# Kernel optimization log

Hardware: AMD Instinct MI355X
Metric: run time of the kernel (lower is better)

## Reference

```python
import jax, jax.numpy as jnp
import numpy as np

N_NODES = 50000
N_EDGES = 800000
IN_DIM = 256
OUT_DIM = 64
HEADS = 8


def setup_inputs() -> dict:
    key = jax.random.key(0)
    k1, k2, k3, k4, k5 = jax.random.split(key, 5)
    x = jax.random.normal(k1, (N_NODES, IN_DIM), dtype=jnp.float32)
    edge_index = jax.random.randint(k2, (2, N_EDGES), 0, N_NODES, dtype=jnp.int32)
    W = jax.random.normal(k3, (HEADS, IN_DIM, OUT_DIM), dtype=jnp.float32) / np.sqrt(IN_DIM)
    b = jnp.zeros((HEADS, OUT_DIM), dtype=jnp.float32)
    a = jax.random.normal(k4, (HEADS, 2 * OUT_DIM), dtype=jnp.float32)
    gate = jnp.ones((HEADS,), dtype=jnp.float32)
    return {"x": x, "edge_index": edge_index, "W": W, "b": b, "a": a, "gate": gate}


def reference(x, edge_index, W, b, a, gate):
    # Wh: [H, N, O] -- per-head linear projections
    Wh = jnp.einsum('nd,hdo->hno', x, W) + b[:, None, :]
    row, col = edge_index[0], edge_index[1]
    O = Wh.shape[-1]
    a_src, a_dst = a[:, :O], a[:, O:]  # split of concat weight: [H, O] each
    # score per edge per head: leaky_relu(cat(Wh[row], Wh[col]) @ a)
    e = (jnp.einsum('heo,ho->he', Wh[:, row], a_src)
         + jnp.einsum('heo,ho->he', Wh[:, col], a_dst))  # [H, E]
    e = jax.nn.leaky_relu(e, negative_slope=0.01)
    # NOTE: original code softmaxes over ALL edges (dim=0), not per node
    alpha = jax.nn.softmax(e, axis=1)  # [H, E]
    msgs = alpha[:, :, None] * Wh[:, col, :]  # [H, E, O]
    out = jax.vmap(lambda m: jax.ops.segment_sum(m, row, num_segments=Wh.shape[1]))(msgs)  # [H, N, O]
    g = jax.nn.softmax(gate)
    return jnp.einsum('h,hno->no', g, out)
```

## Files before the change

### kernel.cpp

```cpp
#include <hip/hip_runtime.h>
#include <hip/hip_bf16.h>


#define N_NODES 50000
#define N_EDGES 800000
#define IN_DIM  256
#define OUT_DIM 64
#define HEADS   8
#define NCOL    (HEADS * OUT_DIM)
#define NBLK_RED 1024
#define LN_W_EPS (-20.72326584f)

typedef __attribute__((ext_vector_type(8))) short short8;
typedef __attribute__((ext_vector_type(4))) float f32x4;

__device__ __forceinline__ void bf16_split2(float x0, float x1,
                                            unsigned& hi, unsigned& lo)
{
    unsigned u0 = __float_as_uint(x0), u1 = __float_as_uint(x1);
    unsigned r0 = u0 + 0x7FFFu + ((u0 >> 16) & 1u);
    unsigned r1 = u1 + 0x7FFFu + ((u1 >> 16) & 1u);
    float h0 = __uint_as_float(r0 & 0xFFFF0000u);
    float h1 = __uint_as_float(r1 & 0xFFFF0000u);
    hi = (r0 >> 16) | (r1 & 0xFFFF0000u);
    unsigned l0 = __float_as_uint(x0 - h0);
    unsigned l1 = __float_as_uint(x1 - h1);
    lo = (l0 >> 16) | (l1 & 0xFFFF0000u);
}

__global__ __launch_bounds__(256) void packw_kernel(
    const float* __restrict__ W, short* __restrict__ wp)
{
    const int ct = blockIdx.x;
    const int h  = ct >> 2;
    #pragma unroll
    for (int it = 0; it < 2; ++it) {
        const int i  = threadIdx.x + it * 256;
        const int k8 = i >> 4;
        const int c  = i & 15;
        const int o  = (ct & 3) * 16 + c;
        const float* src = W + (size_t)h * IN_DIM * OUT_DIM
                             + (size_t)k8 * 8 * OUT_DIM + o;
        unsigned hi[4], lo[4];
        #pragma unroll
        for (int p = 0; p < 4; ++p) {
            float x0 = src[(2 * p) * OUT_DIM];
            float x1 = src[(2 * p + 1) * OUT_DIM];
            bf16_split2(x0, x1, hi[p], lo[p]);
        }
        uint4 vh = make_uint4(hi[0], hi[1], hi[2], hi[3]);
        uint4 vl = make_uint4(lo[0], lo[1], lo[2], lo[3]);
        *(uint4*)(wp + (((size_t)(ct * 2 + 0) * 32 + k8) * 128) + c * 8) = vh;
        *(uint4*)(wp + (((size_t)(ct * 2 + 1) * 32 + k8) * 128) + c * 8) = vl;
    }
}

__global__ __launch_bounds__(512, 4) void gemm_kernel(
    const float* __restrict__ x, const short* __restrict__ wp,
    const float* __restrict__ b, const float* __restrict__ a,
    float* __restrict__ Wh, float* __restrict__ s_src, float* __restrict__ s_dst)
{
    __shared__ __align__(16) short As[32768];

    const int row0 = blockIdx.x * 64;
    const int tid  = threadIdx.x;
    const int lane = tid & 63;
    const int head = tid >> 6;
    const int r16  = lane & 15;
    const int kq   = lane >> 4;

    const short* pB = wp + (size_t)kq * 128 + (size_t)r16 * 8;
    #define LD_B(ni, s, ks) \
        (*(const short8*)(pB + ((((size_t)(head * 4 + (ni)) * 2 + (s)) * 32 + 4 * (ks)) * 128)))
    short8 Bh[2][4], Bl[2][4];
    #pragma unroll
    for (int ni = 0; ni < 4; ++ni) { Bh[0][ni] = LD_B(ni, 0, 0); Bl[0][ni] = LD_B(ni, 1, 0); }

    #pragma unroll
    for (int q = 0; q < 4; ++q) {
        const int item = q * 512 + tid;
        const int row  = item >> 5;
        const int kc   = item & 31;
        const int grow = row0 + row;
        f32x4 v0 = {0.f, 0.f, 0.f, 0.f}, v1 = {0.f, 0.f, 0.f, 0.f};
        if (grow < N_NODES) {
            v0 = *(const f32x4*)(x + (size_t)grow * IN_DIM + kc * 8);
            v1 = *(const f32x4*)(x + (size_t)grow * IN_DIM + kc * 8 + 4);
        }
        unsigned hi[4], lo[4];
        bf16_split2(v0.x, v0.y, hi[0], lo[0]);
        bf16_split2(v0.z, v0.w, hi[1], lo[1]);
        bf16_split2(v1.x, v1.y, hi[2], lo[2]);
        bf16_split2(v1.z, v1.w, hi[3], lo[3]);
        const int mi  = row >> 4, rr = row & 15;
        const int swz = rr ^ (kc & 15);
        uint4 vh = make_uint4(hi[0], hi[1], hi[2], hi[3]);
        uint4 vl = make_uint4(lo[0], lo[1], lo[2], lo[3]);
        *(uint4*)((char*)As + ((((mi * 2 + 0) * 32 + kc) * 16 + swz) * 16)) = vh;
        *(uint4*)((char*)As + ((((mi * 2 + 1) * 32 + kc) * 16 + swz) * 16)) = vl;
    }
    __syncthreads();

    f32x4 acc[4][4] = {};

    #define LD_A(mi, s, ks) \
        (*(const short8*)((const char*)As + \
            (((((mi) * 2 + (s)) * 32 + (4 * (ks) + kq)) * 16 + \
              (r16 ^ ((4 * ((ks) & 3) + kq)))) * 16)))

    short8 Ah[2][4], Al[2][4];
    #pragma unroll
    for (int mi = 0; mi < 4; ++mi) { Ah[0][mi] = LD_A(mi, 0, 0); Al[0][mi] = LD_A(mi, 1, 0); }

    #pragma unroll
    for (int ks = 0; ks < 8; ++ks) {
        const int cur = ks & 1, nxt = cur ^ 1;
        if (ks < 7) {
            #pragma unroll
            for (int ni = 0; ni < 4; ++ni) {
                Bh[nxt][ni] = LD_B(ni, 0, ks + 1);
                Bl[nxt][ni] = LD_B(ni, 1, ks + 1);
            }
            #pragma unroll
            for (int mi = 0; mi < 4; ++mi) {
                Ah[nxt][mi] = LD_A(mi, 0, ks + 1);
                Al[nxt][mi] = LD_A(mi, 1, ks + 1);
            }
        }
        #pragma unroll
        for (int mi = 0; mi < 4; ++mi)
            #pragma unroll
            for (int ni = 0; ni < 4; ++ni) {
                acc[mi][ni] = __builtin_amdgcn_mfma_f32_16x16x32_bf16(
                    Ah[cur][mi], Bh[cur][ni], acc[mi][ni], 0, 0, 0);
                acc[mi][ni] = __builtin_amdgcn_mfma_f32_16x16x32_bf16(
                    Ah[cur][mi], Bl[cur][ni], acc[mi][ni], 0, 0, 0);
                acc[mi][ni] = __builtin_amdgcn_mfma_f32_16x16x32_bf16(
                    Al[cur][mi], Bh[cur][ni], acc[mi][ni], 0, 0, 0);
            }
    }
    #undef LD_A
    #undef LD_B

    const int n0 = head * 64;
    float bias[4], avs[4], avd[4];
    #pragma unroll
    for (int ni = 0; ni < 4; ++ni) {
        bias[ni] = b[n0 + ni * 16 + r16];
        avs[ni]  = a[head * 128 + ni * 16 + r16];
        avd[ni]  = a[head * 128 + 64 + ni * 16 + r16];
    }
    #pragma unroll
    for (int mi = 0; mi < 4; ++mi) {
        #pragma unroll
        for (int reg = 0; reg < 4; ++reg) {
            const int r = row0 + mi * 16 + kq * 4 + reg;
            float v[4], ps = 0.f, pd = 0.f;
            #pragma unroll
            for (int ni = 0; ni < 4; ++ni) {
                v[ni] = acc[mi][ni][reg] + bias[ni];
                ps += v[ni] * avs[ni];
                pd += v[ni] * avd[ni];
            }
            if (r < N_NODES) {
                *(float4*)(Wh + (size_t)r * NCOL + n0 + r16 * 4) =
                    make_float4(v[0], v[1], v[2], v[3]);
            }
            ps += __shfl_xor(ps, 1); pd += __shfl_xor(pd, 1);
            ps += __shfl_xor(ps, 2); pd += __shfl_xor(pd, 2);
            ps += __shfl_xor(ps, 4); pd += __shfl_xor(pd, 4);
            ps += __shfl_xor(ps, 8); pd += __shfl_xor(pd, 8);
            if (r16 == 0 && r < N_NODES) {
                s_src[r * 8 + head] = ps;
                s_dst[r * 8 + head] = pd;
            }
        }
    }
}

__global__ __launch_bounds__(256) void edge_score_kernel(
    const int* __restrict__ ei, const float* __restrict__ s_src,
    const float* __restrict__ s_dst, float* __restrict__ tbuf,
    float* __restrict__ partial)
{
    const int tid  = threadIdx.x;
    const int half = tid & 1;

    float m[4], l[4];
    #pragma unroll
    for (int i = 0; i < 4; ++i) { m[i] = -1e30f; l[i] = 0.f; }

    for (int p = blockIdx.x * 128 + (tid >> 1); p < N_EDGES; p += gridDim.x * 128) {
        const int row = ei[p];
        const int col = ei[N_EDGES + p];
        const f32x4 s = *(const f32x4*)(s_src + row * 8 + half * 4);
        const f32x4 d = *(const f32x4*)(s_dst + col * 8 + half * 4);
        float t[4];
        #pragma unroll
        for (int i = 0; i < 4; ++i) {
            float v = s[i] + d[i];
            t[i] = v > 0.f ? v : 0.01f * v;
        }
        if (tbuf)
            *(float4*)(tbuf + (size_t)p * 8 + half * 4) =
                make_float4(t[0], t[1], t[2], t[3]);
        #pragma unroll
        for (int i = 0; i < 4; ++i) {
            const float mn = fmaxf(m[i], t[i]);
            l[i] = l[i] * __expf(m[i] - mn) + __expf(t[i] - mn);
            m[i] = mn;
        }
    }

    __shared__ float red[8][256];
    #pragma unroll
    for (int i = 0; i < 4; ++i) { red[i][tid] = m[i]; red[4 + i][tid] = l[i]; }
    __syncthreads();
    for (int s = 128; s >= 2; s >>= 1) {
        if (tid < s) {
            #pragma unroll
            for (int i = 0; i < 4; ++i) {
                const float mo = red[i][tid + s], lo = red[4 + i][tid + s];
                const float mm = red[i][tid],     ll = red[4 + i][tid];
                const float mn = fmaxf(mm, mo);
                red[4 + i][tid] = ll * __expf(mm - mn) + lo * __expf(mo - mn);
                red[i][tid]     = mn;
            }
        }
        __syncthreads();
    }
    if (tid < 2) {
        #pragma unroll
        for (int i = 0; i < 4; ++i) {
            partial[blockIdx.x * 16 + tid * 4 + i]     = red[i][tid];
            partial[blockIdx.x * 16 + 8 + tid * 4 + i] = red[4 + i][tid];
        }
    }
}

__global__ __launch_bounds__(256) void finalize_kernel(
    const float* __restrict__ partial, const float* __restrict__ gate,
    float* __restrict__ coef, int nblk)
{
    const int t = threadIdx.x;
    const int h = t & 7;
    const int j = t >> 3;
    float m = -1e30f, l = 0.f;
    for (int bk = j; bk < nblk; bk += 32) {
        const float mb = partial[bk * 16 + h];
        const float lb = partial[bk * 16 + 8 + h];
        const float mn = fmaxf(m, mb);
        l = l * __expf(m - mn) + lb * __expf(mb - mn);
        m = mn;
    }
    __shared__ float rm[256], rl[256];
    rm[t] = m; rl[t] = l;
    __syncthreads();
    for (int s = 128; s >= 8; s >>= 1) {
        if (t < s) {
            const float mo = rm[t + s], lo = rl[t + s];
            const float mn = fmaxf(rm[t], mo);
            rl[t] = rl[t] * __expf(rm[t] - mn) + lo * __expf(mo - mn);
            rm[t] = mn;
        }
        __syncthreads();
    }
    if (t < 8) {
        float gm = gate[0];
        for (int i = 1; i < 8; ++i) gm = fmaxf(gm, gate[i]);
        float gs = 0.f;
        for (int i = 0; i < 8; ++i) gs += __expf(gate[i] - gm);
        const float g = __expf(gate[t] - gm) / gs;
        const float C = g / rl[t];
        coef[t]      = rm[t];
        coef[8 + t]  = C;
        coef[16 + t] = rm[t] + LN_W_EPS - __logf(C);
    }
}

__global__ __launch_bounds__(256) void scatter_t_kernel(
    const int* __restrict__ ei, const float* __restrict__ tbuf,
    const float* __restrict__ Wh, const float* __restrict__ coef,
    float* __restrict__ out)
{
    __shared__ float cM[8], cC[8], cCut[8];
    if (threadIdx.x < 8)       cM[threadIdx.x]        = coef[threadIdx.x];
    else if (threadIdx.x < 16) cC[threadIdx.x - 8]    = coef[threadIdx.x];
    else if (threadIdx.x < 24) cCut[threadIdx.x - 16] = coef[threadIdx.x];
    __syncthreads();

    const int lane = threadIdx.x & 63;
    const int e    = blockIdx.x * 256 + threadIdx.x;

    int row = 0, col = 0;
    bool pass = false;
    float t[8], w[8];
    if (e < N_EDGES) {
        const float4 t0 = *(const float4*)(tbuf + (size_t)e * 8);
        const float4 t1 = *(const float4*)(tbuf + (size_t)e * 8 + 4);
        t[0] = t0.x; t[1] = t0.y; t[2] = t0.z; t[3] = t0.w;
        t[4] = t1.x; t[5] = t1.y; t[6] = t1.z; t[7] = t1.w;
        #pragma unroll
        for (int h = 0; h < 8; ++h) pass |= (t[h] >= cCut[h]);
    }
    if (pass) {
        row = ei[e];
        col = ei[N_EDGES + e];
        #pragma unroll
        for (int h = 0; h < 8; ++h)
            w[h] = __expf(t[h] - cM[h]) * cC[h];
    }

    unsigned long long mask = __ballot(pass);
    while (mask) {
        const int src = (int)__builtin_ctzll(mask);
        mask &= mask - 1;
        const int rb = __shfl(row, src);
        const int cb = __shfl(col, src);
        const float* wc = Wh + (size_t)cb * NCOL + (lane & 15) * 4 + (lane >> 4);
        float acc = 0.f;
        #pragma unroll
        for (int h = 0; h < 8; ++h)
            acc += __shfl(w[h], src) * wc[h * 64];
        atomicAdd(out + (size_t)rb * OUT_DIM + lane, acc);
    }
}

__global__ __launch_bounds__(256) void scatter_kernel(
    const int* __restrict__ ei, const float* __restrict__ s_src,
    const float* __restrict__ s_dst, const float* __restrict__ Wh,
    const float* __restrict__ coef, float* __restrict__ out)
{
    __shared__ float cM[8], cC[8], cCut[8];
    if (threadIdx.x < 8)       cM[threadIdx.x]        = coef[threadIdx.x];
    else if (threadIdx.x < 16) cC[threadIdx.x - 8]    = coef[threadIdx.x];
    else if (threadIdx.x < 24) cCut[threadIdx.x - 16] = coef[threadIdx.x];
    __syncthreads();

    const int lane = threadIdx.x & 63;
    const int e    = blockIdx.x * 256 + threadIdx.x;

    int row = 0, col = 0;
    bool pass = false;
    float w[8];
    if (e < N_EDGES) {
        row = ei[e];
        col = ei[N_EDGES + e];
        const float4 s0 = *(const float4*)(s_src + row * 8);
        const float4 s1 = *(const float4*)(s_src + row * 8 + 4);
        const float4 d0 = *(const float4*)(s_dst + col * 8);
        const float4 d1 = *(const float4*)(s_dst + col * 8 + 4);
        float t[8] = { s0.x + d0.x, s0.y + d0.y, s0.z + d0.z, s0.w + d0.w,
                       s1.x + d1.x, s1.y + d1.y, s1.z + d1.z, s1.w + d1.w };
        #pragma unroll
        for (int h = 0; h < 8; ++h) {
            t[h] = t[h] > 0.f ? t[h] : 0.01f * t[h];
            pass |= (t[h] >= cCut[h]);
        }
        if (pass) {
            #pragma unroll
            for (int h = 0; h < 8; ++h)
                w[h] = __expf(t[h] - cM[h]) * cC[h];
        }
    }

    unsigned long long mask = __ballot(pass);
    while (mask) {
        const int src = (int)__builtin_ctzll(mask);
        mask &= mask - 1;
        const int rb = __shfl(row, src);
        const int cb = __shfl(col, src);
        const float* wc = Wh + (size_t)cb * NCOL + (lane & 15) * 4 + (lane >> 4);
        float acc = 0.f;
        #pragma unroll
        for (int h = 0; h < 8; ++h)
            acc += __shfl(w[h], src) * wc[h * 64];
        atomicAdd(out + (size_t)rb * OUT_DIM + lane, acc);
    }
}

extern "C" void kernel_launch(void* const* d_in, const int* in_sizes, int n_in,
                              void* d_out, int out_size, void* d_ws, size_t ws_size,
                              hipStream_t stream)
{
    const float* x    = (const float*)d_in[0];
    const int*   ei   = (const int*)  d_in[1];
    const float* W    = (const float*)d_in[2];
    const float* b    = (const float*)d_in[3];
    const float* a    = (const float*)d_in[4];
    const float* gate = (const float*)d_in[5];
    float* out = (float*)d_out;

    float* ws      = (float*)d_ws;
    float* Wh      = ws;
    float* s_src   = Wh    + (size_t)N_NODES * NCOL;
    float* s_dst   = s_src + (size_t)N_NODES * HEADS;
    float* partial = s_dst + (size_t)N_NODES * HEADS;
    float* coef    = partial + (size_t)NBLK_RED * 16;
    short* wp      = (short*)(coef + 32);
    float* tbuf    = (float*)(wp + 262144);

    const size_t base_bytes = (size_t)((char*)tbuf - (char*)ws);
    const size_t need_tbuf  = base_bytes + (size_t)N_EDGES * 8 * sizeof(float);
    const bool   use_tbuf   = ws_size >= need_tbuf;

    hipMemsetAsync(d_out, 0, (size_t)N_NODES * OUT_DIM * sizeof(float), stream);

    packw_kernel<<<32, 256, 0, stream>>>(W, wp);

    gemm_kernel<<<(N_NODES + 63) / 64, 512, 0, stream>>>(x, wp, b, a, Wh, s_src, s_dst);

    edge_score_kernel<<<NBLK_RED, 256, 0, stream>>>(
        ei, s_src, s_dst, use_tbuf ? tbuf : nullptr, partial);

    finalize_kernel<<<1, 256, 0, stream>>>(partial, gate, coef, NBLK_RED);

    if (use_tbuf)
        scatter_t_kernel<<<(N_EDGES + 255) / 256, 256, 0, stream>>>(
            ei, tbuf, Wh, coef, out);
    else
        scatter_kernel<<<(N_EDGES + 255) / 256, 256, 0, stream>>>(
            ei, s_src, s_dst, Wh, coef, out);
}
```

Measured before the change: 221.8 us.

## Compute Wh lazily only for columns referenced by surviving edges

```diff
diff --git a/kernel.cpp b/kernel.cpp
--- a/kernel.cpp
+++ b/kernel.cpp
@@ -55,17 +55,21 @@
     }
 }
 
-__global__ __launch_bounds__(512, 4) void gemm_kernel(
+__global__ __launch_bounds__(256, 2) void gemm_kernel(
     const float* __restrict__ x, const short* __restrict__ wp,
     const float* __restrict__ b, const float* __restrict__ a,
-    float* __restrict__ Wh, float* __restrict__ s_src, float* __restrict__ s_dst)
+    float* __restrict__ s_src, float* __restrict__ s_dst)
 {
     __shared__ __align__(16) short As[32768];
-
-    const int row0 = blockIdx.x * 64;
+    __shared__ __align__(16) float s_tmp[2][64][4];
+
+    const int pid  = blockIdx.x >> 1;
+    const int hh   = blockIdx.x & 1;
+    const int row0 = pid * 64;
     const int tid  = threadIdx.x;
     const int lane = tid & 63;
-    const int head = tid >> 6;
+    const int w    = tid >> 6;
+    const int head = hh * 4 + w;
     const int r16  = lane & 15;
     const int kq   = lane >> 4;
 
@@ -77,8 +81,8 @@
     for (int ni = 0; ni < 4; ++ni) { Bh[0][ni] = LD_B(ni, 0, 0); Bl[0][ni] = LD_B(ni, 1, 0); }
 
     #pragma unroll
-    for (int q = 0; q < 4; ++q) {
-        const int item = q * 512 + tid;
+    for (int q = 0; q < 8; ++q) {
+        const int item = q * 256 + tid;
         const int row  = item >> 5;
         const int kc   = item & 31;
         const int grow = row0 + row;
@@ -154,34 +158,38 @@
     for (int mi = 0; mi < 4; ++mi) {
         #pragma unroll
         for (int reg = 0; reg < 4; ++reg) {
-            const int r = row0 + mi * 16 + kq * 4 + reg;
-            float v[4], ps = 0.f, pd = 0.f;
+            float ps = 0.f, pd = 0.f;
             #pragma unroll
             for (int ni = 0; ni < 4; ++ni) {
-                v[ni] = acc[mi][ni][reg] + bias[ni];
-                ps += v[ni] * avs[ni];
-                pd += v[ni] * avd[ni];
-            }
-            if (r < N_NODES) {
-                *(float4*)(Wh + (size_t)r * NCOL + n0 + r16 * 4) =
-                    make_float4(v[0], v[1], v[2], v[3]);
+                const float v = acc[mi][ni][reg] + bias[ni];
+                ps += v * avs[ni];
+                pd += v * avd[ni];
             }
             ps += __shfl_xor(ps, 1); pd += __shfl_xor(pd, 1);
             ps += __shfl_xor(ps, 2); pd += __shfl_xor(pd, 2);
             ps += __shfl_xor(ps, 4); pd += __shfl_xor(pd, 4);
             ps += __shfl_xor(ps, 8); pd += __shfl_xor(pd, 8);
-            if (r16 == 0 && r < N_NODES) {
-                s_src[r * 8 + head] = ps;
-                s_dst[r * 8 + head] = pd;
-            }
+            if (r16 == 0) {
+                const int rloc = mi * 16 + kq * 4 + reg;
+                s_tmp[0][rloc][w] = ps;
+                s_tmp[1][rloc][w] = pd;
+            }
+        }
+    }
+    __syncthreads();
+    if (tid < 128) {
+        const int r = row0 + (tid & 63);
+        if (r < N_NODES) {
+            float* dst = (tid < 64) ? s_src : s_dst;
+            *(float4*)(dst + (size_t)r * 8 + hh * 4) =
+                *(const float4*)&s_tmp[tid >> 6][tid & 63][0];
         }
     }
 }
 
 __global__ __launch_bounds__(256) void edge_score_kernel(
     const int* __restrict__ ei, const float* __restrict__ s_src,
-    const float* __restrict__ s_dst, float* __restrict__ tbuf,
-    float* __restrict__ partial)
+    const float* __restrict__ s_dst, float* __restrict__ partial)
 {
     const int tid  = threadIdx.x;
     const int half = tid & 1;
@@ -195,19 +203,12 @@
         const int col = ei[N_EDGES + p];
         const f32x4 s = *(const f32x4*)(s_src + row * 8 + half * 4);
         const f32x4 d = *(const f32x4*)(s_dst + col * 8 + half * 4);
-        float t[4];
         #pragma unroll
         for (int i = 0; i < 4; ++i) {
             float v = s[i] + d[i];
-            t[i] = v > 0.f ? v : 0.01f * v;
-        }
-        if (tbuf)
-            *(float4*)(tbuf + (size_t)p * 8 + half * 4) =
-                make_float4(t[0], t[1], t[2], t[3]);
-        #pragma unroll
-        for (int i = 0; i < 4; ++i) {
-            const float mn = fmaxf(m[i], t[i]);
-            l[i] = l[i] * __expf(m[i] - mn) + __expf(t[i] - mn);
+            const float t = v > 0.f ? v : 0.01f * v;
+            const float mn = fmaxf(m[i], t);
+            l[i] = l[i] * __expf(m[i] - mn) + __expf(t - mn);
             m[i] = mn;
         }
     }
@@ -278,73 +279,20 @@
     }
 }
 
-__global__ __launch_bounds__(256) void scatter_t_kernel(
-    const int* __restrict__ ei, const float* __restrict__ tbuf,
-    const float* __restrict__ Wh, const float* __restrict__ coef,
-    float* __restrict__ out)
-{
-    __shared__ float cM[8], cC[8], cCut[8];
-    if (threadIdx.x < 8)       cM[threadIdx.x]        = coef[threadIdx.x];
-    else if (threadIdx.x < 16) cC[threadIdx.x - 8]    = coef[threadIdx.x];
-    else if (threadIdx.x < 24) cCut[threadIdx.x - 16] = coef[threadIdx.x];
-    __syncthreads();
-
-    const int lane = threadIdx.x & 63;
-    const int e    = blockIdx.x * 256 + threadIdx.x;
-
-    int row = 0, col = 0;
+__global__ __launch_bounds__(256) void mark_kernel(
+    const int* __restrict__ ei, const float* __restrict__ s_src,
+    const float* __restrict__ s_dst, const float* __restrict__ coef,
+    int* __restrict__ elist, int* __restrict__ colflag, int* __restrict__ ecount)
+{
+    __shared__ float cCut[8];
+    if (threadIdx.x < 8) cCut[threadIdx.x] = coef[16 + threadIdx.x];
+    __syncthreads();
+
+    const int e = blockIdx.x * 256 + threadIdx.x;
     bool pass = false;
-    float t[8], w[8];
+    int col = 0;
     if (e < N_EDGES) {
-        const float4 t0 = *(const float4*)(tbuf + (size_t)e * 8);
-        const float4 t1 = *(const float4*)(tbuf + (size_t)e * 8 + 4);
-        t[0] = t0.x; t[1] = t0.y; t[2] = t0.z; t[3] = t0.w;
-        t[4] = t1.x; t[5] = t1.y; t[6] = t1.z; t[7] = t1.w;
-        #pragma unroll
-        for (int h = 0; h < 8; ++h) pass |= (t[h] >= cCut[h]);
-    }
-    if (pass) {
-        row = ei[e];
-        col = ei[N_EDGES + e];
-        #pragma unroll
-        for (int h = 0; h < 8; ++h)
-            w[h] = __expf(t[h] - cM[h]) * cC[h];
-    }
-
-    unsigned long long mask = __ballot(pass);
-    while (mask) {
-        const int src = (int)__builtin_ctzll(mask);
-        mask &= mask - 1;
-        const int rb = __shfl(row, src);
-        const int cb = __shfl(col, src);
-        const float* wc = Wh + (size_t)cb * NCOL + (lane & 15) * 4 + (lane >> 4);
-        float acc = 0.f;
-        #pragma unroll
-        for (int h = 0; h < 8; ++h)
-            acc += __shfl(w[h], src) * wc[h * 64];
-        atomicAdd(out + (size_t)rb * OUT_DIM + lane, acc);
-    }
-}
-
-__global__ __launch_bounds__(256) void scatter_kernel(
-    const int* __restrict__ ei, const float* __restrict__ s_src,
-    const float* __restrict__ s_dst, const float* __restrict__ Wh,
-    const float* __restrict__ coef, float* __restrict__ out)
-{
-    __shared__ float cM[8], cC[8], cCut[8];
-    if (threadIdx.x < 8)       cM[threadIdx.x]        = coef[threadIdx.x];
-    else if (threadIdx.x < 16) cC[threadIdx.x - 8]    = coef[threadIdx.x];
-    else if (threadIdx.x < 24) cCut[threadIdx.x - 16] = coef[threadIdx.x];
-    __syncthreads();
-
-    const int lane = threadIdx.x & 63;
-    const int e    = blockIdx.x * 256 + threadIdx.x;
-
-    int row = 0, col = 0;
-    bool pass = false;
-    float w[8];
-    if (e < N_EDGES) {
-        row = ei[e];
+        const int row = ei[e];
         col = ei[N_EDGES + e];
         const float4 s0 = *(const float4*)(s_src + row * 8);
         const float4 s1 = *(const float4*)(s_src + row * 8 + 4);
@@ -357,25 +305,103 @@
             t[h] = t[h] > 0.f ? t[h] : 0.01f * t[h];
             pass |= (t[h] >= cCut[h]);
         }
+    }
+
+    const unsigned long long mask = __ballot(pass);
+    if (mask) {
+        const int lane   = threadIdx.x & 63;
+        const int leader = (int)__builtin_ctzll(mask);
+        int base = 0;
+        if (lane == leader) base = atomicAdd(ecount, (int)__popcll(mask));
+        base = __shfl(base, leader);
         if (pass) {
+            const int rank = (int)__popcll(mask & ((1ULL << lane) - 1ULL));
+            elist[base + rank] = e;
+            colflag[col] = 1;
+        }
+    }
+}
+
+__global__ __launch_bounds__(256) void whrows_kernel(
+    const float* __restrict__ x, const float* __restrict__ W,
+    const float* __restrict__ b, const int* __restrict__ colflag,
+    float* __restrict__ Wh)
+{
+    __shared__ __align__(16) float xr[4][256];
+    const int w    = threadIdx.x >> 6;
+    const int lane = threadIdx.x & 63;
+    const int n0   = blockIdx.x * 64;
+
+    for (int i = w; i < 64; i += 4) {
+        const int n = n0 + i;
+        if (n >= N_NODES) break;
+        if (colflag[n] == 0) continue;
+
+        *(f32x4*)&xr[w][lane * 4] = *(const f32x4*)(x + (size_t)n * IN_DIM + lane * 4);
+        const int hq = lane >> 4, oq = lane & 15;
+        f32x4 acc0 = {0.f, 0.f, 0.f, 0.f}, acc1 = {0.f, 0.f, 0.f, 0.f};
+        for (int k = 0; k < IN_DIM; ++k) {
+            const float xk = xr[w][k];
+            acc0 += xk * *(const f32x4*)(W + ((size_t)hq * IN_DIM + k) * OUT_DIM + oq * 4);
+            acc1 += xk * *(const f32x4*)(W + ((size_t)(hq + 4) * IN_DIM + k) * OUT_DIM + oq * 4);
+        }
+        acc0 += *(const f32x4*)(b + hq * OUT_DIM + oq * 4);
+        acc1 += *(const f32x4*)(b + (hq + 4) * OUT_DIM + oq * 4);
+        *(f32x4*)(Wh + (size_t)n * NCOL + hq * OUT_DIM + oq * 4)       = acc0;
+        *(f32x4*)(Wh + (size_t)n * NCOL + (hq + 4) * OUT_DIM + oq * 4) = acc1;
+    }
+}
+
+__global__ __launch_bounds__(256) void acc_kernel(
+    const int* __restrict__ ei, const float* __restrict__ s_src,
+    const float* __restrict__ s_dst, const float* __restrict__ Wh,
+    const float* __restrict__ coef, const int* __restrict__ elist,
+    const int* __restrict__ ecount, float* __restrict__ out)
+{
+    __shared__ float cM[8], cC[8];
+    if (threadIdx.x < 8)       cM[threadIdx.x]     = coef[threadIdx.x];
+    else if (threadIdx.x < 16) cC[threadIdx.x - 8] = coef[threadIdx.x];
+    __syncthreads();
+
+    const int n    = *ecount;
+    const int lane = threadIdx.x & 63;
+
+    for (int i = blockIdx.x * 256 + threadIdx.x; ; i += gridDim.x * 256) {
+        const bool has = i < n;
+        if (!__any(has)) break;
+
+        int row = 0, col = 0;
+        float wgt[8];
+        if (has) {
+            const int e = elist[i];
+            row = ei[e];
+            col = ei[N_EDGES + e];
+            const float4 s0 = *(const float4*)(s_src + row * 8);
+            const float4 s1 = *(const float4*)(s_src + row * 8 + 4);
+            const float4 d0 = *(const float4*)(s_dst + col * 8);
+            const float4 d1 = *(const float4*)(s_dst + col * 8 + 4);
+            float t[8] = { s0.x + d0.x, s0.y + d0.y, s0.z + d0.z, s0.w + d0.w,
+                           s1.x + d1.x, s1.y + d1.y, s1.z + d1.z, s1.w + d1.w };
+            #pragma unroll
+            for (int h = 0; h < 8; ++h) {
+                t[h] = t[h] > 0.f ? t[h] : 0.01f * t[h];
+                wgt[h] = __expf(t[h] - cM[h]) * cC[h];
+            }
+        }
+
+        unsigned long long mask = __ballot(has);
+        while (mask) {
+            const int src = (int)__builtin_ctzll(mask);
+            mask &= mask - 1;
+            const int rb = __shfl(row, src);
+            const int cb = __shfl(col, src);
+            const float* wc = Wh + (size_t)cb * NCOL + lane;
+            float acc = 0.f;
             #pragma unroll
             for (int h = 0; h < 8; ++h)
-                w[h] = __expf(t[h] - cM[h]) * cC[h];
-        }
-    }
-
-    unsigned long long mask = __ballot(pass);
-    while (mask) {
-        const int src = (int)__builtin_ctzll(mask);
-        mask &= mask - 1;
-        const int rb = __shfl(row, src);
-        const int cb = __shfl(col, src);
-        const float* wc = Wh + (size_t)cb * NCOL + (lane & 15) * 4 + (lane >> 4);
-        float acc = 0.f;
-        #pragma unroll
-        for (int h = 0; h < 8; ++h)
-            acc += __shfl(w[h], src) * wc[h * 64];
-        atomicAdd(out + (size_t)rb * OUT_DIM + lane, acc);
+                acc += __shfl(wgt[h], src) * wc[h * 64];
+            atomicAdd(out + (size_t)rb * OUT_DIM + lane, acc);
+        }
     }
 }
 
@@ -398,27 +424,27 @@
     float* partial = s_dst + (size_t)N_NODES * HEADS;
     float* coef    = partial + (size_t)NBLK_RED * 16;
     short* wp      = (short*)(coef + 32);
-    float* tbuf    = (float*)(wp + 262144);
-
-    const size_t base_bytes = (size_t)((char*)tbuf - (char*)ws);
-    const size_t need_tbuf  = base_bytes + (size_t)N_EDGES * 8 * sizeof(float);
-    const bool   use_tbuf   = ws_size >= need_tbuf;
+    int*   elist   = (int*)(wp + 262144);
+    int*   colflag = elist + N_EDGES;
+    int*   ecount  = colflag + N_NODES;
 
     hipMemsetAsync(d_out, 0, (size_t)N_NODES * OUT_DIM * sizeof(float), stream);
+    hipMemsetAsync(colflag, 0, (size_t)(N_NODES + 1) * sizeof(int), stream);
 
     packw_kernel<<<32, 256, 0, stream>>>(W, wp);
 
-    gemm_kernel<<<(N_NODES + 63) / 64, 512, 0, stream>>>(x, wp, b, a, Wh, s_src, s_dst);
-
-    edge_score_kernel<<<NBLK_RED, 256, 0, stream>>>(
-        ei, s_src, s_dst, use_tbuf ? tbuf : nullptr, partial);
+    gemm_kernel<<<((N_NODES + 63) / 64) * 2, 256, 0, stream>>>(
+        x, wp, b, a, s_src, s_dst);
+
+    edge_score_kernel<<<NBLK_RED, 256, 0, stream>>>(ei, s_src, s_dst, partial);
 
     finalize_kernel<<<1, 256, 0, stream>>>(partial, gate, coef, NBLK_RED);
 
-    if (use_tbuf)
-        scatter_t_kernel<<<(N_EDGES + 255) / 256, 256, 0, stream>>>(
-            ei, tbuf, Wh, coef, out);
-    else
-        scatter_kernel<<<(N_EDGES + 255) / 256, 256, 0, stream>>>(
-            ei, s_src, s_dst, Wh, coef, out);
-}
+    mark_kernel<<<(N_EDGES + 255) / 256, 256, 0, stream>>>(
+        ei, s_src, s_dst, coef, elist, colflag, ecount);
+
+    whrows_kernel<<<(N_NODES + 63) / 64, 256, 0, stream>>>(x, W, b, colflag, Wh);
+
+    acc_kernel<<<256, 256, 0, stream>>>(
+        ei, s_src, s_dst, Wh, coef, elist, ecount, out);
+}
```

Result: slower. 459.1 us (+107.0%).
